# Performance work log

Measured on AMD Instinct MI355X. Metric: run time of the kernel, lower is better.

## Reference

```python
import jax, jax.numpy as jnp
import numpy as np

B, LV, LL, LO, E, H = 8, 1024, 1024, 512, 768, 12


def setup_inputs() -> dict:
    key = jax.random.key(0)
    ks = jax.random.split(key, 8)
    w_scale = 0.02
    return {
        "V": jax.random.normal(ks[0], (B, LV, E), jnp.float32),
        "L": jax.random.normal(ks[1], (B, LL, E), jnp.float32),
        "O": jax.random.normal(ks[2], (B, LO, E), jnp.float32),
        "attn_mask": jax.random.normal(ks[3], (LO, LV + LL), jnp.float32) * 0.1,
        "in_w1": jax.random.normal(ks[4], (3 * E, E), jnp.float32) * w_scale,
        "in_b1": jnp.zeros((3 * E,), jnp.float32),
        "in_w2": jax.random.normal(ks[5], (3 * E, E), jnp.float32) * w_scale,
        "in_b2": jnp.zeros((3 * E,), jnp.float32),
        "out_w": jax.random.normal(ks[6], (E, E), jnp.float32) * w_scale,
        "out_b": jnp.zeros((E,), jnp.float32),
    }


def reference(V, L, O, attn_mask, in_w1, in_b1, in_w2, in_b2, out_w, out_b):
    num_heads = H
    b, lo, e = O.shape
    lv, ll = V.shape[1], L.shape[1]
    d = e // num_heads
    scale = 1.0 / jnp.sqrt(jnp.float32(d))

    wq1, wk1, wv1 = jnp.split(in_w1, 3, axis=0)
    bq1, bk1, bv1 = jnp.split(in_b1, 3, axis=0)
    wq2, wk2, wv2 = jnp.split(in_w2, 3, axis=0)
    bq2, bk2, bv2 = jnp.split(in_b2, 3, axis=0)

    # projections, split into heads: [b, t, h, d]
    q1 = (O @ wq1.T + bq1).reshape(b, lo, num_heads, d)
    q2 = (O @ wq2.T + bq2).reshape(b, lo, num_heads, d)
    k1 = (V @ wk1.T + bk1).reshape(b, lv, num_heads, d)
    v1 = (V @ wv1.T + bv1).reshape(b, lv, num_heads, d)
    k2 = (L @ wk2.T + bk2).reshape(b, ll, num_heads, d)
    v2 = (L @ wv2.T + bv2).reshape(b, ll, num_heads, d)

    # dual-source scores, additive float mask sliced per source
    s1 = jnp.einsum('bthd,bshd->bhts', q1, k1) * scale + attn_mask[:, :lv]
    s2 = jnp.einsum('bthd,bshd->bhts', q2, k2) * scale + attn_mask[:, lv:lv + ll]

    attn = jax.nn.softmax(jnp.concatenate([s1, s2], axis=-1), axis=-1)  # [b,h,t,lv+ll]
    v_cat = jnp.concatenate([v1, v2], axis=1)  # [b, lv+ll, h, d]
    ctx = jnp.einsum('bhts,bshd->bthd', attn, v_cat).reshape(b, lo, e)

    out = ctx @ out_w.T + out_b  # [b, lo, e]
    attn_avg = attn.mean(axis=1)  # average over heads: [b, lo, lv+ll]
    return out, attn_avg
```

## Files before the change

kernel.cpp:

```cpp
#include <hip/hip_runtime.h>
#include <hip/hip_bf16.h>
#include <type_traits>

#define B_  8
#define LO_ 512
#define E_  768
#define H_  12
#define S_  2048

typedef __attribute__((ext_vector_type(8))) short bf16x8;
typedef __attribute__((ext_vector_type(4))) float f32x4;
#define MFMA16(a,b,c) __builtin_amdgcn_mfma_f32_16x16x32_bf16(a, b, c, 0, 0, 0)

__device__ inline short f2bf(float f) {
  __hip_bfloat16 h = __float2bfloat16(f);
  return *reinterpret_cast<short*>(&h);
}
__device__ inline float bf2f(short s) {
  unsigned int u = ((unsigned int)(unsigned short)s) << 16;
  return __uint_as_float(u);
}

template <typename TC>
__global__ __launch_bounds__(256) void gemm_mfma(
    const float* __restrict__ A, const float* __restrict__ W,
    const float* __restrict__ bias, TC* __restrict__ C, int R)
{
  constexpr int N = 768, K = 768;
  __shared__ short As[64*72] __attribute__((aligned(16)));
  __shared__ short Ws[64*72] __attribute__((aligned(16)));
  const int tid = threadIdx.x, wv = tid >> 6, lane = tid & 63;
  const int quad = lane >> 4, l15 = lane & 15;
  const int r0 = blockIdx.x * 64, c0 = blockIdx.y * 64;
  const int srow = tid >> 2, sk = (tid & 3) * 16;

  f32x4 acc[4] = {};

  for (int k0 = 0; k0 < K; k0 += 64) {
    float a16[16], w16[16];
    const float4* ga = (const float4*)(A + (size_t)(r0 + srow) * K + k0 + sk);
    const float4* gw = (const float4*)(W + (size_t)(c0 + srow) * K + k0 + sk);
#pragma unroll
    for (int i = 0; i < 4; ++i) {
      float4 va = ga[i]; a16[4*i] = va.x; a16[4*i+1] = va.y; a16[4*i+2] = va.z; a16[4*i+3] = va.w;
      float4 vw = gw[i]; w16[4*i] = vw.x; w16[4*i+1] = vw.y; w16[4*i+2] = vw.z; w16[4*i+3] = vw.w;
    }
    bf16x8 pa[2], pw[2];
#pragma unroll
    for (int g = 0; g < 2; ++g)
#pragma unroll
      for (int i = 0; i < 8; ++i) { pa[g][i] = f2bf(a16[g*8+i]); pw[g][i] = f2bf(w16[g*8+i]); }
    __syncthreads();
    *(bf16x8*)&As[srow*72 + sk]     = pa[0];
    *(bf16x8*)&As[srow*72 + sk + 8] = pa[1];
    *(bf16x8*)&Ws[srow*72 + sk]     = pw[0];
    *(bf16x8*)&Ws[srow*72 + sk + 8] = pw[1];
    __syncthreads();

    bf16x8 af0 = *(const bf16x8*)&As[(wv*16 + l15)*72 +      quad*8];
    bf16x8 af1 = *(const bf16x8*)&As[(wv*16 + l15)*72 + 32 + quad*8];
#pragma unroll
    for (int ct = 0; ct < 4; ++ct) {
      bf16x8 bf0 = *(const bf16x8*)&Ws[(ct*16 + l15)*72 +      quad*8];
      bf16x8 bf1 = *(const bf16x8*)&Ws[(ct*16 + l15)*72 + 32 + quad*8];
      acc[ct] = MFMA16(af0, bf0, acc[ct]);
      acc[ct] = MFMA16(af1, bf1, acc[ct]);
    }
  }

#pragma unroll
  for (int ct = 0; ct < 4; ++ct) {
    const int col = c0 + ct*16 + l15;
    const float bv = bias[col];
#pragma unroll
    for (int r = 0; r < 4; ++r) {
      const int row = r0 + wv*16 + quad*4 + r;
      const float v = acc[ct][r] + bv;
      if constexpr (std::is_same_v<TC, float>) C[(size_t)row * N + col] = v;
      else                                     C[(size_t)row * N + col] = __float2bfloat16(v);
    }
  }
}

__device__ __forceinline__ void stats_load(
    const __hip_bfloat16* __restrict__ kq, const float* __restrict__ mb, int it,
    bf16x8 (&kb)[4][2], float (&mv)[4][4])
{
#pragma unroll
  for (int ct = 0; ct < 4; ++ct) {
    kb[ct][0] = *(const bf16x8*)(kq + (size_t)ct*16*E_);
    kb[ct][1] = *(const bf16x8*)(kq + (size_t)ct*16*E_ + 32);
#pragma unroll
    for (int r = 0; r < 4; ++r)
      mv[ct][r] = mb[(size_t)r*S_ + it*256 + ct*16];
  }
}

__device__ __forceinline__ void stats_compute(
    const bf16x8 (&qa)[2], const bf16x8 (&kb)[4][2], const float (&mv)[4][4],
    float (&m_l)[4], float (&l_l)[4])
{
  float v[4][4];
#pragma unroll
  for (int ct = 0; ct < 4; ++ct) {
    f32x4 sacc = {};
    sacc = MFMA16(qa[0], kb[ct][0], sacc);
    sacc = MFMA16(qa[1], kb[ct][1], sacc);
#pragma unroll
    for (int r = 0; r < 4; ++r) v[ct][r] = sacc[r]*0.125f + mv[ct][r];
  }
#pragma unroll
  for (int r = 0; r < 4; ++r) {
    const float cm = fmaxf(fmaxf(v[0][r], v[1][r]), fmaxf(v[2][r], v[3][r]));
    const float mn = fmaxf(m_l[r], cm);
    const float add = (__expf(v[0][r]-mn) + __expf(v[1][r]-mn))
                    + (__expf(v[2][r]-mn) + __expf(v[3][r]-mn));
    l_l[r] = l_l[r]*__expf(m_l[r]-mn) + add;
    m_l[r] = mn;
  }
}

__global__ __launch_bounds__(256) void attn_stats(
    const __hip_bfloat16* __restrict__ q1, const __hip_bfloat16* __restrict__ q2,
    const __hip_bfloat16* __restrict__ k1, const __hip_bfloat16* __restrict__ k2,
    const float* __restrict__ mask, float* __restrict__ stats)
{
  __shared__ float smm[4][16], sml[4][16];

  const int tid = threadIdx.x, wv = tid >> 6, lane = tid & 63;
  const int quad = lane >> 4, l15 = lane & 15;
  const int bid = blockIdx.x;
  const int Lid = (bid & 7) * 384 + (bid >> 3);
  const int qt = Lid & 31, h = (Lid >> 5) % 12, b = Lid / 384;
  const int r0 = qt * 16;

  bf16x8 qa0[2], qa1[2];
#pragma unroll
  for (int ks = 0; ks < 2; ++ks) {
    qa0[ks] = *(const bf16x8*)(q1 + ((size_t)(b*LO_ + r0 + l15))*E_ + h*64 + ks*32 + quad*8);
    qa1[ks] = *(const bf16x8*)(q2 + ((size_t)(b*LO_ + r0 + l15))*E_ + h*64 + ks*32 + quad*8);
  }

  const float* mb = mask + (size_t)(r0 + quad*4)*S_ + wv*64 + l15;
  const __hip_bfloat16* kp1 = k1 + ((size_t)(b*1024 + wv*64 + l15))*E_ + h*64 + quad*8;
  const __hip_bfloat16* kp2 = k2 + ((size_t)(b*1024 + wv*64 + l15))*E_ + h*64 + quad*8;

  float m_l[4] = {-3.0e38f, -3.0e38f, -3.0e38f, -3.0e38f};
  float l_l[4] = {};

  bf16x8 kA[4][2], kB[4][2];
  float  mA[4][4], mB[4][4];

  stats_load(kp1 + (size_t)0*256*E_, mb, 0, kA, mA);
  stats_load(kp1 + (size_t)1*256*E_, mb, 1, kB, mB);
  stats_compute(qa0, kA, mA, m_l, l_l);
  stats_load(kp1 + (size_t)2*256*E_, mb, 2, kA, mA);
  stats_compute(qa0, kB, mB, m_l, l_l);
  stats_load(kp1 + (size_t)3*256*E_, mb, 3, kB, mB);
  stats_compute(qa0, kA, mA, m_l, l_l);
  stats_load(kp2 + (size_t)0*256*E_, mb, 4, kA, mA);
  stats_compute(qa0, kB, mB, m_l, l_l);
  stats_load(kp2 + (size_t)1*256*E_, mb, 5, kB, mB);
  stats_compute(qa1, kA, mA, m_l, l_l);
  stats_load(kp2 + (size_t)2*256*E_, mb, 6, kA, mA);
  stats_compute(qa1, kB, mB, m_l, l_l);
  stats_load(kp2 + (size_t)3*256*E_, mb, 7, kB, mB);
  stats_compute(qa1, kA, mA, m_l, l_l);
  stats_compute(qa1, kB, mB, m_l, l_l);

#pragma unroll
  for (int off = 1; off < 16; off <<= 1) {
#pragma unroll
    for (int r = 0; r < 4; ++r) {
      const float mo = __shfl_xor(m_l[r], off, 64);
      const float lo = __shfl_xor(l_l[r], off, 64);
      const float mn = fmaxf(m_l[r], mo);
      l_l[r] = l_l[r]*__expf(m_l[r]-mn) + lo*__expf(mo-mn);
      m_l[r] = mn;
    }
  }
  if (l15 == 0) {
#pragma unroll
    for (int r = 0; r < 4; ++r) { smm[wv][quad*4+r] = m_l[r]; sml[wv][quad*4+r] = l_l[r]; }
  }
  __syncthreads();
  if (tid < 16) {
    float m = smm[0][tid], l = sml[0][tid];
#pragma unroll
    for (int ww = 1; ww < 4; ++ww) {
      const float mo = smm[ww][tid], lo = sml[ww][tid];
      const float mn = fmaxf(m, mo);
      l = l*__expf(m-mn) + lo*__expf(mo-mn);
      m = mn;
    }
    const size_t idx = (((size_t)(b*H_ + h))*LO_ + r0 + tid) * 2;
    stats[idx] = m; stats[idx+1] = 1.0f / l;
  }
}

#define OFF_VT   0
#define OFF_PST  17408
#define OFF_OBUF 21760
#define SMEM_MAIN 29952

__global__ __launch_bounds__(512, 4) void attn_main(
    const __hip_bfloat16* __restrict__ q1, const __hip_bfloat16* __restrict__ q2,
    const __hip_bfloat16* __restrict__ k1, const __hip_bfloat16* __restrict__ v1,
    const __hip_bfloat16* __restrict__ k2, const __hip_bfloat16* __restrict__ v2,
    const float* __restrict__ mask, const float* __restrict__ stats,
    float* __restrict__ ctx, float* __restrict__ avg)
{
  extern __shared__ char smem[];
  short* vT   = (short*)(smem + OFF_VT);
  short* pst  = (short*)(smem + OFF_PST);
  float* obuf = (float*)(smem + OFF_OBUF);

  const int tid = threadIdx.x, wv = tid >> 6, lane = tid & 63;
  const int quad = lane >> 4, l15 = lane & 15;
  const int bid = blockIdx.x;
  const int Lid = (bid & 7) * 128 + (bid >> 3);
  const int b = Lid >> 7;
  const int inner = Lid & 127;
  const int src = inner & 1, ks = (inner >> 1) & 1, qt = inner >> 2;
  const int r0 = qt * 16;
  const int kb0 = b*1024 + ks*512;
  const __hip_bfloat16* qws = src ? q2 : q1;
  const __hip_bfloat16* kws = src ? k2 : k1;
  const __hip_bfloat16* vws = src ? v2 : v1;

  const int cpr = wv >> 2;
  const int ct  = wv & 3;
  const int nb  = cpr*64 + ct*16;

  const int vrow = tid >> 2, vc16 = (tid & 3) * 16;
  const int vbase = vc16*136 + (((vrow >> 3) ^ ((tid & 3) << 1)) << 3) + (vrow & 7);
  const int dimv = ct*16 + l15;
  const int vr0 = dimv*136 + (((cpr*8 +     quad) ^ (ct << 1)) << 3);
  const int vr1 = dimv*136 + (((cpr*8 + 4 + quad) ^ (ct << 1)) << 3);

  unsigned int mpk[8];
  {
    const float* mptr = mask + (size_t)(r0 + quad*4)*S_ + src*1024 + ks*512 + nb + l15;
#pragma unroll
    for (int cp = 0; cp < 4; ++cp) {
      const float m0 = mptr[(size_t)0*S_ + cp*128];
      const float m1 = mptr[(size_t)1*S_ + cp*128];
      const float m2 = mptr[(size_t)2*S_ + cp*128];
      const float m3 = mptr[(size_t)3*S_ + cp*128];
      mpk[cp*2]   = (unsigned int)(unsigned short)f2bf(m0) | ((unsigned int)(unsigned short)f2bf(m1) << 16);
      mpk[cp*2+1] = (unsigned int)(unsigned short)f2bf(m2) | ((unsigned int)(unsigned short)f2bf(m3) << 16);
    }
  }

  float pacc[4][4] = {};

  bf16x8 vA0, vA1, vB0, vB1;

#define CP_BODY(CP, VC0, VC1, VN0, VN1)                                              \
  {                                                                                  \
    __syncthreads();                      \
                  \
    const __hip_bfloat16* kp = kws + ((size_t)(kb0 + (CP)*128 + nb + l15))*E_ + h*64 + quad*8; \
    const bf16x8 kc0 = *(const bf16x8*)kp;                                           \
    const bf16x8 kc1 = *(const bf16x8*)(kp + 32);                                    \
    _Pragma("unroll")                                                                \
    for (int i = 0; i < 8; ++i) vT[vbase + i*136]     = VC0[i];                      \
    _Pragma("unroll")                                                                \
    for (int i = 0; i < 8; ++i) vT[vbase + (i+8)*136] = VC1[i];                      \
    if ((CP) < 3) {                                     \
      const bf16x8* gv = (const bf16x8*)(vws + ((size_t)(kb0 + ((CP)+1)*128 + vrow))*E_ + h*64 + vc16); \
      VN0 = gv[0]; VN1 = gv[1];                                                      \
    }                                                                                \
    {                                                                                \
      f32x4 sacc = {};                                                               \
      sacc = MFMA16(qa0, kc0, sacc);                                                 \
      sacc = MFMA16(qa1, kc1, sacc);                                                 \
      const unsigned int w0 = mpk[(CP)*2], w1 = mpk[(CP)*2+1];                       \
      float mr[4];                                                                   \
      mr[0] = bf2f((short)(w0 & 0xffff)); mr[1] = bf2f((short)(w0 >> 16));           \
      mr[2] = bf2f((short)(w1 & 0xffff)); mr[3] = bf2f((short)(w1 >> 16));           \
      _Pragma("unroll")                                                              \
      for (int r = 0; r < 4; ++r) {                                                  \
        const float p = __expf(sacc[r]*0.125f + mr[r] - m_r[r]) * il_r[r];           \
        pacc[CP][r] += p;                                                            \
        pst[(quad*4 + r)*136 + nb + l15] = f2bf(p);                                  \
      }                                                                              \
    }                                                                                \
    __syncthreads();                                           \
    {                                                                                \
      const bf16x8 pa0 = *(const bf16x8*)&pst[l15*136 + cpr*64 +      quad*8];       \
      const bf16x8 pa1 = *(const bf16x8*)&pst[l15*136 + cpr*64 + 32 + quad*8];       \
      const bf16x8 vb0 = *(const bf16x8*)&vT[vr0];                                   \
      const bf16x8 vb1 = *(const bf16x8*)&vT[vr1];                                   \
      oacc = MFMA16(pa0, vb0, oacc);                                                 \
      oacc = MFMA16(pa1, vb1, oacc);                                                 \
    }                                                                                \
  }

#pragma unroll 1
  for (int h = 0; h < H_; ++h) {
    const __hip_bfloat16* qp = qws + ((size_t)(b*LO_ + r0 + l15))*E_ + h*64 + quad*8;
    const bf16x8 qa0 = *(const bf16x8*)qp;
    const bf16x8 qa1 = *(const bf16x8*)(qp + 32);

    float m_r[4], il_r[4];
#pragma unroll
    for (int r = 0; r < 4; ++r) {
      const size_t idx = (((size_t)(b*H_ + h))*LO_ + r0 + quad*4 + r) * 2;
      m_r[r] = stats[idx]; il_r[r] = stats[idx+1];
    }

    {
      const bf16x8* gv = (const bf16x8*)(vws + ((size_t)(kb0 + vrow))*E_ + h*64 + vc16);
      vA0 = gv[0]; vA1 = gv[1];
    }

    f32x4 oacc = {};

    CP_BODY(0, vA0, vA1, vB0, vB1)
    CP_BODY(1, vB0, vB1, vA0, vA1)
    CP_BODY(2, vA0, vA1, vB0, vB1)
    CP_BODY(3, vB0, vB1, vA0, vA1)

    __syncthreads();
#pragma unroll
    for (int r = 0; r < 4; ++r) obuf[wv*256 + r*64 + lane] = oacc[r];
    __syncthreads();
#pragma unroll
    for (int e0 = 0; e0 < 2; ++e0) {
      const int e = tid + e0*512;
      const int row = e >> 6, dim = e & 63;
      const int idx = (row & 3)*64 + (row >> 2)*16 + (dim & 15);
      const float v = obuf[(dim >> 4)*256 + idx] + obuf[((dim >> 4) + 4)*256 + idx];
      atomicAdd(&ctx[((size_t)(b*LO_ + r0 + row))*E_ + h*64 + dim], v);
    }
  }
#undef CP_BODY

  {
    constexpr float invH = 1.0f / 12.0f;
#pragma unroll
    for (int cp = 0; cp < 4; ++cp)
#pragma unroll
      for (int r = 0; r < 4; ++r)
        avg[(size_t)(b*LO_ + r0 + quad*4 + r)*S_ + src*1024 + ks*512 + cp*128 + nb + l15]
            = pacc[cp][r] * invH;
  }
}

extern "C" void kernel_launch(void* const* d_in, const int* in_sizes, int n_in,
                              void* d_out, int out_size, void* d_ws, size_t ws_size,
                              hipStream_t stream) {
  const float* V    = (const float*)d_in[0];
  const float* Lm   = (const float*)d_in[1];
  const float* O    = (const float*)d_in[2];
  const float* mask = (const float*)d_in[3];
  const float* w1   = (const float*)d_in[4];
  const float* b1   = (const float*)d_in[5];
  const float* w2   = (const float*)d_in[6];
  const float* b2   = (const float*)d_in[7];
  const float* ow   = (const float*)d_in[8];
  const float* ob   = (const float*)d_in[9];
  float* out = (float*)d_out;

  __hip_bfloat16* ws  = (__hip_bfloat16*)d_ws;
  __hip_bfloat16* q1  = ws;
  __hip_bfloat16* q2  = q1 + (size_t)4096*768;
  __hip_bfloat16* k1  = q2 + (size_t)4096*768;
  __hip_bfloat16* v1  = k1 + (size_t)8192*768;
  __hip_bfloat16* k2  = v1 + (size_t)8192*768;
  __hip_bfloat16* v2  = k2 + (size_t)8192*768;
  float* ctx   = (float*)(v2 + (size_t)8192*768);
  float* stats = ctx + (size_t)4096*768;

  hipMemsetAsync(ctx, 0, (size_t)4096*768*4, stream);

  dim3 blk(256);
  gemm_mfma<__hip_bfloat16><<<dim3(64, 12),  blk, 0, stream>>>(O,  w1,             b1,        q1, 4096);
  gemm_mfma<__hip_bfloat16><<<dim3(64, 12),  blk, 0, stream>>>(O,  w2,             b2,        q2, 4096);
  gemm_mfma<__hip_bfloat16><<<dim3(128, 12), blk, 0, stream>>>(V,  w1 + 768*768,   b1 + 768,  k1, 8192);
  gemm_mfma<__hip_bfloat16><<<dim3(128, 12), blk, 0, stream>>>(V,  w1 + 2*768*768, b1 + 1536, v1, 8192);
  gemm_mfma<__hip_bfloat16><<<dim3(128, 12), blk, 0, stream>>>(Lm, w2 + 768*768,   b2 + 768,  k2, 8192);
  gemm_mfma<__hip_bfloat16><<<dim3(128, 12), blk, 0, stream>>>(Lm, w2 + 2*768*768, b2 + 1536, v2, 8192);

  attn_stats<<<dim3(3072), blk, 0, stream>>>(q1, q2, k1, k2, mask, stats);

  hipFuncSetAttribute((const void*)attn_main, hipFuncAttributeMaxDynamicSharedMemorySize, SMEM_MAIN);
  attn_main<<<dim3(1024), dim3(512), SMEM_MAIN, stream>>>(q1, q2, k1, v1, k2, v2, mask, stats,
                                                          ctx, out + (size_t)4096*768);

  gemm_mfma<float><<<dim3(64, 12), blk, 0, stream>>>(ctx, ow, ob, out, 4096);
}
```

Baseline: 651.1 us.

## Pre-convert inputs and weights to bf16 and use 128-row GEMM tiles

Adds a standalone fp32-to-bf16 conversion kernel. Weights and activations (V, L, O, ctx) are converted once before the projection GEMMs, so V and L are converted once instead of once per K/V GEMM, and the GEMMs now read bf16 directly. The GEMM tile grows to 128 rows so each W fragment feeds twice as many MFMAs. It also reuses the ctx buffer as scratch for the converted activations before ctx is zeroed. The cost is extra conversion launches and an extra round trip through memory for each converted tensor.

New measurement: 543.6 us. 1.2x faster.

```diff
diff --git a/kernel.cpp b/kernel.cpp
--- a/kernel.cpp
+++ b/kernel.cpp
@@ -21,50 +21,66 @@
   return __uint_as_float(u);
 }
 
+__global__ __launch_bounds__(256) void to_bf16(
+    const float* __restrict__ in, __hip_bfloat16* __restrict__ out, int n8)
+{
+  const int i = blockIdx.x * 256 + threadIdx.x;
+  if (i >= n8) return;
+  const float4* p = (const float4*)(in + (size_t)i * 8);
+  const float4 a = p[0], b = p[1];
+  short r[8] = { f2bf(a.x), f2bf(a.y), f2bf(a.z), f2bf(a.w),
+                 f2bf(b.x), f2bf(b.y), f2bf(b.z), f2bf(b.w) };
+  *(bf16x8*)(out + (size_t)i * 8) = *(bf16x8*)r;
+}
+
 template <typename TC>
-__global__ __launch_bounds__(256) void gemm_mfma(
-    const float* __restrict__ A, const float* __restrict__ W,
+__global__ __launch_bounds__(256) void gemm_bf16(
+    const __hip_bfloat16* __restrict__ A, const __hip_bfloat16* __restrict__ W,
     const float* __restrict__ bias, TC* __restrict__ C, int R)
 {
   constexpr int N = 768, K = 768;
-  __shared__ short As[64*72] __attribute__((aligned(16)));
-  __shared__ short Ws[64*72] __attribute__((aligned(16)));
+  __shared__ short As[128*72] __attribute__((aligned(16)));
+  __shared__ short Ws[64*72]  __attribute__((aligned(16)));
   const int tid = threadIdx.x, wv = tid >> 6, lane = tid & 63;
   const int quad = lane >> 4, l15 = lane & 15;
-  const int r0 = blockIdx.x * 64, c0 = blockIdx.y * 64;
-  const int srow = tid >> 2, sk = (tid & 3) * 16;
-
-  f32x4 acc[4] = {};
+  const int r0 = blockIdx.x * 128, c0 = blockIdx.y * 64;
+  const int arow = tid >> 1, aks = (tid & 1) * 32;
+  const int wrow = tid >> 2, wks = (tid & 3) * 16;
+
+  f32x4 acc[2][4] = {};
 
   for (int k0 = 0; k0 < K; k0 += 64) {
-    float a16[16], w16[16];
-    const float4* ga = (const float4*)(A + (size_t)(r0 + srow) * K + k0 + sk);
-    const float4* gw = (const float4*)(W + (size_t)(c0 + srow) * K + k0 + sk);
-#pragma unroll
-    for (int i = 0; i < 4; ++i) {
-      float4 va = ga[i]; a16[4*i] = va.x; a16[4*i+1] = va.y; a16[4*i+2] = va.z; a16[4*i+3] = va.w;
-      float4 vw = gw[i]; w16[4*i] = vw.x; w16[4*i+1] = vw.y; w16[4*i+2] = vw.z; w16[4*i+3] = vw.w;
-    }
-    bf16x8 pa[2], pw[2];
-#pragma unroll
-    for (int g = 0; g < 2; ++g)
-#pragma unroll
-      for (int i = 0; i < 8; ++i) { pa[g][i] = f2bf(a16[g*8+i]); pw[g][i] = f2bf(w16[g*8+i]); }
+    const __hip_bfloat16* ga = A + (size_t)(r0 + arow) * K + k0 + aks;
+    const __hip_bfloat16* gw = W + (size_t)(c0 + wrow) * K + k0 + wks;
+    const bf16x8 a0 = *(const bf16x8*)ga;
+    const bf16x8 a1 = *(const bf16x8*)(ga + 8);
+    const bf16x8 a2 = *(const bf16x8*)(ga + 16);
+    const bf16x8 a3 = *(const bf16x8*)(ga + 24);
+    const bf16x8 w0 = *(const bf16x8*)gw;
+    const bf16x8 w1 = *(const bf16x8*)(gw + 8);
     __syncthreads();
-    *(bf16x8*)&As[srow*72 + sk]     = pa[0];
-    *(bf16x8*)&As[srow*72 + sk + 8] = pa[1];
-    *(bf16x8*)&Ws[srow*72 + sk]     = pw[0];
-    *(bf16x8*)&Ws[srow*72 + sk + 8] = pw[1];
+    *(bf16x8*)&As[arow*72 + aks]      = a0;
+    *(bf16x8*)&As[arow*72 + aks + 8]  = a1;
+    *(bf16x8*)&As[arow*72 + aks + 16] = a2;
+    *(bf16x8*)&As[arow*72 + aks + 24] = a3;
+    *(bf16x8*)&Ws[wrow*72 + wks]      = w0;
+    *(bf16x8*)&Ws[wrow*72 + wks + 8]  = w1;
     __syncthreads();
 
-    bf16x8 af0 = *(const bf16x8*)&As[(wv*16 + l15)*72 +      quad*8];
-    bf16x8 af1 = *(const bf16x8*)&As[(wv*16 + l15)*72 + 32 + quad*8];
+    bf16x8 af[2][2];
+#pragma unroll
+    for (int s = 0; s < 2; ++s)
+#pragma unroll
+      for (int kk = 0; kk < 2; ++kk)
+        af[s][kk] = *(const bf16x8*)&As[(s*64 + wv*16 + l15)*72 + kk*32 + quad*8];
 #pragma unroll
     for (int ct = 0; ct < 4; ++ct) {
-      bf16x8 bf0 = *(const bf16x8*)&Ws[(ct*16 + l15)*72 +      quad*8];
-      bf16x8 bf1 = *(const bf16x8*)&Ws[(ct*16 + l15)*72 + 32 + quad*8];
-      acc[ct] = MFMA16(af0, bf0, acc[ct]);
-      acc[ct] = MFMA16(af1, bf1, acc[ct]);
+      const bf16x8 bf0 = *(const bf16x8*)&Ws[(ct*16 + l15)*72 +      quad*8];
+      const bf16x8 bf1 = *(const bf16x8*)&Ws[(ct*16 + l15)*72 + 32 + quad*8];
+      acc[0][ct] = MFMA16(af[0][0], bf0, acc[0][ct]);
+      acc[0][ct] = MFMA16(af[0][1], bf1, acc[0][ct]);
+      acc[1][ct] = MFMA16(af[1][0], bf0, acc[1][ct]);
+      acc[1][ct] = MFMA16(af[1][1], bf1, acc[1][ct]);
     }
   }
 
@@ -73,12 +89,14 @@
     const int col = c0 + ct*16 + l15;
     const float bv = bias[col];
 #pragma unroll
-    for (int r = 0; r < 4; ++r) {
-      const int row = r0 + wv*16 + quad*4 + r;
-      const float v = acc[ct][r] + bv;
-      if constexpr (std::is_same_v<TC, float>) C[(size_t)row * N + col] = v;
-      else                                     C[(size_t)row * N + col] = __float2bfloat16(v);
-    }
+    for (int s = 0; s < 2; ++s)
+#pragma unroll
+      for (int r = 0; r < 4; ++r) {
+        const int row = r0 + s*64 + wv*16 + quad*4 + r;
+        const float v = acc[s][ct][r] + bv;
+        if constexpr (std::is_same_v<TC, float>) C[(size_t)row * N + col] = v;
+        else                                     C[(size_t)row * N + col] = __float2bfloat16(v);
+      }
   }
 }
 
@@ -372,16 +390,30 @@
   __hip_bfloat16* v2  = k2 + (size_t)8192*768;
   float* ctx   = (float*)(v2 + (size_t)8192*768);
   float* stats = ctx + (size_t)4096*768;
+  __hip_bfloat16* w1b  = (__hip_bfloat16*)(stats + (size_t)8*12*512*2);
+  __hip_bfloat16* w2b  = w1b + (size_t)3*768*768;
+  __hip_bfloat16* owb  = w2b + (size_t)3*768*768;
+  __hip_bfloat16* ctxb = owb + (size_t)768*768;
+  __hip_bfloat16* scr  = (__hip_bfloat16*)ctx;
+
+  dim3 blk(256);
+  const int W8 = 768*768/8;
+
+  to_bf16<<<dim3((3*W8 + 255)/256), blk, 0, stream>>>(w1, w1b, 3*W8);
+  to_bf16<<<dim3((3*W8 + 255)/256), blk, 0, stream>>>(w2, w2b, 3*W8);
+  to_bf16<<<dim3((W8   + 255)/256), blk, 0, stream>>>(ow, owb, W8);
+
+  to_bf16<<<dim3(8192*768/8/256), blk, 0, stream>>>(V, scr, 8192*768/8);
+  gemm_bf16<__hip_bfloat16><<<dim3(64, 12), blk, 0, stream>>>(scr, w1b +   768*768, b1 + 768,  k1, 8192);
+  gemm_bf16<__hip_bfloat16><<<dim3(64, 12), blk, 0, stream>>>(scr, w1b + 2*768*768, b1 + 1536, v1, 8192);
+  to_bf16<<<dim3(8192*768/8/256), blk, 0, stream>>>(Lm, scr, 8192*768/8);
+  gemm_bf16<__hip_bfloat16><<<dim3(64, 12), blk, 0, stream>>>(scr, w2b +   768*768, b2 + 768,  k2, 8192);
+  gemm_bf16<__hip_bfloat16><<<dim3(64, 12), blk, 0, stream>>>(scr, w2b + 2*768*768, b2 + 1536, v2, 8192);
+  to_bf16<<<dim3(4096*768/8/256), blk, 0, stream>>>(O, scr, 4096*768/8);
+  gemm_bf16<__hip_bfloat16><<<dim3(32, 12), blk, 0, stream>>>(scr, w1b, b1, q1, 4096);
+  gemm_bf16<__hip_bfloat16><<<dim3(32, 12), blk, 0, stream>>>(scr, w2b, b2, q2, 4096);
 
   hipMemsetAsync(ctx, 0, (size_t)4096*768*4, stream);
-
-  dim3 blk(256);
-  gemm_mfma<__hip_bfloat16><<<dim3(64, 12),  blk, 0, stream>>>(O,  w1,             b1,        q1, 4096);
-  gemm_mfma<__hip_bfloat16><<<dim3(64, 12),  blk, 0, stream>>>(O,  w2,             b2,        q2, 4096);
-  gemm_mfma<__hip_bfloat16><<<dim3(128, 12), blk, 0, stream>>>(V,  w1 + 768*768,   b1 + 768,  k1, 8192);
-  gemm_mfma<__hip_bfloat16><<<dim3(128, 12), blk, 0, stream>>>(V,  w1 + 2*768*768, b1 + 1536, v1, 8192);
-  gemm_mfma<__hip_bfloat16><<<dim3(128, 12), blk, 0, stream>>>(Lm, w2 + 768*768,   b2 + 768,  k2, 8192);
-  gemm_mfma<__hip_bfloat16><<<dim3(128, 12), blk, 0, stream>>>(Lm, w2 + 2*768*768, b2 + 1536, v2, 8192);
 
   attn_stats<<<dim3(3072), blk, 0, stream>>>(q1, q2, k1, k2, mask, stats);
 
@@ -389,5 +421,6 @@
   attn_main<<<dim3(1024), dim3(512), SMEM_MAIN, stream>>>(q1, q2, k1, v1, k2, v2, mask, stats,
                                                           ctx, out + (size_t)4096*768);
 
-  gemm_mfma<float><<<dim3(64, 12), blk, 0, stream>>>(ctx, ow, ob, out, 4096);
-}
+  to_bf16<<<dim3(4096*768/8/256), blk, 0, stream>>>(ctx, ctxb, 4096*768/8);
+  gemm_bf16<float><<<dim3(32, 12), blk, 0, stream>>>(ctxb, owb, ob, out, 4096);
+}
```
